# Kernel tuning notes

Hardware: AMD Instinct MI355X
Metric: run time of the kernel (lower is better)

## Reference

```python
import jax, jax.numpy as jnp
import numpy as np

B, N, D = 8, 256, 128   # batch, nodes, feature width
MID, OUT = 128, 128
FEAT = 2 * D            # concat(n_features, hidden)


def _glorot(key, fan_in, fan_out):
    s = (2.0 / (fan_in + fan_out)) ** 0.5
    return jax.random.normal(key, (fan_in, fan_out), dtype=jnp.float32) * s


def setup_inputs() -> dict:
    key = jax.random.key(0)
    ks = jax.random.split(key, 12)
    inp = {
        "hidden": jax.random.normal(ks[0], (B, N, D), dtype=jnp.float32),
        "n_features": jax.random.normal(ks[1], (B, N, D), dtype=jnp.float32),
        "e_features": jax.random.normal(ks[2], (B, N, N, D), dtype=jnp.float32),
        "g_features": jax.random.normal(ks[3], (B, D), dtype=jnp.float32),
        "adj": jax.random.bernoulli(ks[4], 0.5, (B, N, N)).astype(jnp.float32),
        # Linear params (haiku Linear: y = x @ w + b)
        "W1": _glorot(ks[5], FEAT, MID), "b1": jnp.zeros((MID,), jnp.float32),
        "W2": _glorot(ks[6], FEAT, MID), "b2": jnp.zeros((MID,), jnp.float32),
        "We": _glorot(ks[7], D, MID),    "be": jnp.zeros((MID,), jnp.float32),
        "Wg": _glorot(ks[8], D, MID),    "bg": jnp.zeros((MID,), jnp.float32),
        "Wo1": _glorot(ks[9], FEAT, OUT), "bo1": jnp.zeros((OUT,), jnp.float32),
        "Wo2": _glorot(ks[10], MID, OUT), "bo2": jnp.zeros((OUT,), jnp.float32),
    }
    return inp


def reference(hidden, n_features, e_features, g_features, adj,
              W1, b1, W2, b2, We, be, Wg, bg, Wo1, bo1, Wo2, bo2):
    # features: (B, N, 2D)
    features = jnp.concatenate([n_features, hidden], axis=-1)
    msg_1 = features @ W1 + b1              # (B, N, MID)
    msg_2 = features @ W2 + b2              # (B, N, MID)
    msg_e = e_features @ We + be            # (B, N, N, MID)
    msg_g = g_features @ Wg + bg            # (B, MID)
    # broadcast-add: msgs[b, i, j] = msg_1[b, j] + msg_2[b, i] + msg_e[b, i, j] + msg_g[b]
    msgs = (msg_1[:, None, :, :] + msg_2[:, :, None, :]
            + msg_e + msg_g[:, None, None, :])  # (B, N, N, MID)
    # masked max reduction over axis=1 (default reduction=jnp.max branch)
    msgs = jnp.max(msgs * adj[..., None], axis=1)  # (B, N, MID)
    ret = (features @ Wo1 + bo1) + (msgs @ Wo2 + bo2)  # (B, N, OUT)
    return ret
```

## Files before the change

kernel.cpp:

```cpp
#include <hip/hip_runtime.h>
#include <stdint.h>

#define B_   8
#define N_   256
#define D_   128
#define MID_ 128
#define FEAT_ 256

typedef __attribute__((ext_vector_type(4))) float  floatx4;
typedef __attribute__((ext_vector_type(4))) int    intx4;
typedef __attribute__((ext_vector_type(8))) __bf16 bf16x8;

__device__ __forceinline__ floatx4 mfma16(bf16x8 a, bf16x8 b, floatx4 c) {
    return __builtin_amdgcn_mfma_f32_16x16x32_bf16(a, b, c, 0, 0, 0);
}

__device__ __forceinline__ bf16x8 cvt8(floatx4 a, floatx4 b) {
    bf16x8 r;
    r[0] = (__bf16)a[0]; r[1] = (__bf16)a[1]; r[2] = (__bf16)a[2]; r[3] = (__bf16)a[3];
    r[4] = (__bf16)b[0]; r[5] = (__bf16)b[1]; r[6] = (__bf16)b[2]; r[7] = (__bf16)b[3];
    return r;
}

__global__ void __launch_bounds__(256)
kW(const float* __restrict__ W1, const float* __restrict__ W2,
   const float* __restrict__ Wo1, const float* __restrict__ We,
   __bf16* __restrict__ dst) {
    int t = threadIdx.x;
    int g = blockIdx.x * 2 + (t >> 7);
    int m = t & 127;
    const float* src; int kg; int off;
    if (g < 32)      { src = W1;  kg = g;      off = 0; }
    else if (g < 64) { src = W2;  kg = g - 32; off = 32768; }
    else if (g < 96) { src = Wo1; kg = g - 64; off = 65536; }
    else             { src = We;  kg = g - 96; off = 98304; }
    bf16x8 r;
#pragma unroll
    for (int jv = 0; jv < 8; ++jv) r[jv] = (__bf16)src[(kg * 8 + jv) * MID_ + m];
    int base = (((kg >> 2) * 8 + (m >> 4)) * 64 + (kg & 3) * 16 + (m & 15)) * 8;
    *(bf16x8*)&dst[off + base] = r;
}

__global__ void __launch_bounds__(256)
kA(const float* __restrict__ nfeat, const float* __restrict__ hidden,
   const __bf16* __restrict__ Wpre,
   const float* __restrict__ g, const float* __restrict__ Wg,
   const float* __restrict__ bg, const float* __restrict__ b1,
   const float* __restrict__ be, const float* __restrict__ b2,
   const float* __restrict__ bo1, const float* __restrict__ bo2,
   float* __restrict__ C, float* __restrict__ msg2, float* __restrict__ retA) {
    __shared__ __bf16 Wb[8 * 8 * 64 * 8];
    __shared__ float gp_part[2][MID_];
    __shared__ float gp_sh[MID_];
    int t = threadIdx.x;
    int wid = blockIdx.y;
    {
        const intx4* srcW = (const intx4*)(Wpre + (size_t)wid * 32768);
        intx4* dstW = (intx4*)Wb;
#pragma unroll
        for (int it = 0; it < 16; ++it) dstW[t + it * 256] = srcW[t + it * 256];
    }
    int bblk = blockIdx.x >> 2;
    if (wid == 0) {
        int m = t & 127, h = t >> 7;
        const float* gr = g + bblk * D_;
        float a = 0.f;
        for (int k = h * 64; k < h * 64 + 64; ++k)
            a += gr[k] * Wg[k * MID_ + m];
        gp_part[h][m] = a;
    }
    __syncthreads();
    if (wid == 0 && t < 128)
        gp_sh[t] = gp_part[0][t] + gp_part[1][t] + bg[t] + b1[t] + be[t];
    __syncthreads();

    int lane = t & 63, w = t >> 6;
    int n16 = lane & 15, quad = lane >> 4;
    int R = blockIdx.x * 64 + w * 16 + n16;
    const float* frow0 = nfeat  + (size_t)R * D_ + quad * 8;
    const float* frow1 = hidden + (size_t)R * D_ + quad * 8;

    bf16x8 bfrag[8];
#pragma unroll
    for (int ks = 0; ks < 8; ++ks) {
        const float* p = (ks < 4) ? (frow0 + ks * 32) : (frow1 + (ks - 4) * 32);
        floatx4 v0 = *(const floatx4*)p;
        floatx4 v1 = *(const floatx4*)(p + 4);
        bfrag[ks] = cvt8(v0, v1);
    }

    float* outp = (wid == 0) ? C : ((wid == 1) ? msg2 : retA);
#pragma unroll 2
    for (int mt = 0; mt < 8; ++mt) {
        floatx4 acc = (floatx4)0.f;
#pragma unroll
        for (int ks = 0; ks < 8; ++ks) {
            bf16x8 a = *(const bf16x8*)&Wb[((ks * 8 + mt) * 64 + lane) * 8];
            acc = mfma16(a, bfrag[ks], acc);
        }
        int m0 = mt * 16 + quad * 4;
        floatx4 add;
        if (wid == 0)      add = *(const floatx4*)&gp_sh[m0];
        else if (wid == 1) add = *(const floatx4*)&b2[m0];
        else {
            floatx4 x = *(const floatx4*)&bo1[m0];
            floatx4 y = *(const floatx4*)&bo2[m0];
            add = x + y;
        }
        *(floatx4*)&outp[(size_t)R * MID_ + m0] = acc + add;
    }
}

__global__ void __launch_bounds__(256, 4)
kB(const float* __restrict__ e, const __bf16* __restrict__ Wes,
   const float* __restrict__ adj, const float* __restrict__ C,
   const float* __restrict__ msg2, const float* __restrict__ retA,
   const float* __restrict__ Wo2, float* __restrict__ out) {
    __shared__ __bf16 Wb[4 * 8 * 64 * 8];
    __shared__ float C_sh[MID_];
    __shared__ float wmax[4][MID_];
    __shared__ float msgs_sh[MID_];
    __shared__ float part[2][MID_];
    __shared__ unsigned short list_sh[N_];
    __shared__ float aval_sh[N_];
    __shared__ int wcnt[4];

    int t = threadIdx.x;
    int b = blockIdx.x >> 8, j = blockIdx.x & 255;
    int lane = t & 63, w = t >> 6;
    int n16 = lane & 15, quad = lane >> 4;

    {
        const intx4* srcW = (const intx4*)Wes;
        intx4* dstW = (intx4*)Wb;
#pragma unroll
        for (int it = 0; it < 8; ++it) dstW[t + it * 256] = srcW[t + it * 256];
    }
    float av = adj[(size_t)b * N_ * N_ + (size_t)t * N_ + j];
    bool act = (av != 0.f);
    unsigned long long mk = __ballot(act);
    if (lane == 0) wcnt[w] = __popcll(mk);
    if (t < 128) C_sh[t] = C[((size_t)b * N_ + j) * MID_ + t];
    __syncthreads();
    int nact = wcnt[0] + wcnt[1] + wcnt[2] + wcnt[3];
    int base = 0;
    if (w > 0) base += wcnt[0];
    if (w > 1) base += wcnt[1];
    if (w > 2) base += wcnt[2];
    int pos = base + __popcll(mk & ((1ull << lane) - 1ull));
    if (act) { list_sh[pos] = (unsigned short)t; aval_sh[pos] = av; }
    __syncthreads();

    const size_t erow = (size_t)N_ * D_;
    const float* ebase = e + (size_t)b * N_ * N_ * D_ + (size_t)j * D_ + quad * 8;
    const float* m2b   = msg2 + (size_t)b * N_ * MID_;

    floatx4 rm[8];
#pragma unroll
    for (int mt = 0; mt < 8; ++mt) rm[mt] = (floatx4)(-INFINITY);

    int nch = (nact + 15) >> 4;

    int idxn = 0; float awn = 0.f;
    {
        int slot = w * 16 + n16;
        if (w < nch && slot < nact) { idxn = list_sh[slot]; awn = aval_sh[slot]; }
    }
    floatx4 v[8];
    {
        const float* rowp = ebase + (size_t)idxn * erow;
#pragma unroll
        for (int q = 0; q < 4; ++q) {
            v[2 * q]     = *(const floatx4*)(rowp + q * 32);
            v[2 * q + 1] = *(const floatx4*)(rowp + q * 32 + 4);
        }
    }

    for (int c = w; c < nch; c += 4) {
        bf16x8 ef[4];
#pragma unroll
        for (int q = 0; q < 4; ++q) ef[q] = cvt8(v[2 * q], v[2 * q + 1]);
        float aw = awn;
        const float* m2r = m2b + (size_t)idxn * MID_;

        int cn = c + 4;
        idxn = 0; awn = 0.f;
        {
            int slot = cn * 16 + n16;
            if (cn < nch && slot < nact) { idxn = list_sh[slot]; awn = aval_sh[slot]; }
        }
        {
            const float* rowp = ebase + (size_t)idxn * erow;
#pragma unroll
            for (int q = 0; q < 4; ++q) {
                v[2 * q]     = *(const floatx4*)(rowp + q * 32);
                v[2 * q + 1] = *(const floatx4*)(rowp + q * 32 + 4);
            }
        }

#pragma unroll 2
        for (int mt = 0; mt < 8; ++mt) {
            int m0 = mt * 16 + quad * 4;
            floatx4 m2v = *(const floatx4*)&m2r[m0];
            floatx4 acc = *(const floatx4*)&C_sh[m0];
#pragma unroll
            for (int ks = 0; ks < 4; ++ks) {
                bf16x8 aW = *(const bf16x8*)&Wb[((ks * 8 + mt) * 64 + lane) * 8];
                acc = mfma16(aW, ef[ks], acc);
            }
#pragma unroll
            for (int r = 0; r < 4; ++r)
                rm[mt][r] = fmaxf(rm[mt][r], (acc[r] + m2v[r]) * aw);
        }
    }

#pragma unroll
    for (int mt = 0; mt < 8; ++mt) {
#pragma unroll
        for (int r = 0; r < 4; ++r) {
            float vv = rm[mt][r];
            vv = fmaxf(vv, __shfl_xor(vv, 1, 64));
            vv = fmaxf(vv, __shfl_xor(vv, 2, 64));
            vv = fmaxf(vv, __shfl_xor(vv, 4, 64));
            vv = fmaxf(vv, __shfl_xor(vv, 8, 64));
            rm[mt][r] = vv;
        }
    }
    if (n16 == 0) {
#pragma unroll
        for (int mt = 0; mt < 8; ++mt)
            *(floatx4*)&wmax[w][mt * 16 + quad * 4] = rm[mt];
    }
    __syncthreads();

    int m = t & 127, h = t >> 7;
    if (t < 128) {
        float mx = fmaxf(fmaxf(wmax[0][m], wmax[1][m]), fmaxf(wmax[2][m], wmax[3][m]));
        if (nact < 256) mx = fmaxf(mx, 0.f);
        msgs_sh[m] = mx;
    }
    __syncthreads();

    float a2 = 0.f;
    for (int k = h * 64; k < h * 64 + 64; ++k)
        a2 += msgs_sh[k] * Wo2[k * MID_ + m];
    part[h][m] = a2;
    __syncthreads();
    if (t < 128) {
        int R = b * N_ + j;
        out[(size_t)R * MID_ + m] = retA[R * MID_ + m] + part[0][m] + part[1][m];
    }
}

extern "C" void kernel_launch(void* const* d_in, const int* in_sizes, int n_in,
                              void* d_out, int out_size, void* d_ws, size_t ws_size,
                              hipStream_t stream) {
    (void)in_sizes; (void)n_in; (void)out_size; (void)ws_size;
    const float* hidden = (const float*)d_in[0];
    const float* nfeat  = (const float*)d_in[1];
    const float* e      = (const float*)d_in[2];
    const float* g      = (const float*)d_in[3];
    const float* adj    = (const float*)d_in[4];
    const float* W1  = (const float*)d_in[5];
    const float* b1  = (const float*)d_in[6];
    const float* W2  = (const float*)d_in[7];
    const float* b2  = (const float*)d_in[8];
    const float* We  = (const float*)d_in[9];
    const float* be  = (const float*)d_in[10];
    const float* Wg  = (const float*)d_in[11];
    const float* bg  = (const float*)d_in[12];
    const float* Wo1 = (const float*)d_in[13];
    const float* bo1 = (const float*)d_in[14];
    const float* Wo2 = (const float*)d_in[15];
    const float* bo2 = (const float*)d_in[16];
    float* outp = (float*)d_out;

    float* ws = (float*)d_ws;
    __bf16* Wpre = (__bf16*)ws;
    float* C    = ws + 57344;
    float* msg2 = C + 262144;
    float* retA = msg2 + 262144;

    kW<<<56, 256, 0, stream>>>(W1, W2, Wo1, We, Wpre);
    kA<<<dim3(32, 3), 256, 0, stream>>>(nfeat, hidden, Wpre,
                                        g, Wg, bg, b1, be, b2, bo1, bo2,
                                        C, msg2, retA);
    kB<<<2048, 256, 0, stream>>>(e, Wpre + 98304, adj, C, msg2, retA, Wo2, outp);
}
```

Baseline: 399.9 us.

## Restructure edge-chunk loop to pair MFMA chunks and transpose Wo2 for vector loads

```diff
diff --git a/kernel.cpp b/kernel.cpp
--- a/kernel.cpp
+++ b/kernel.cpp
@@ -22,23 +22,70 @@
     return r;
 }
 
+#define LOAD8(v, rp) do { _Pragma("unroll") \
+    for (int q = 0; q < 4; ++q) { \
+        v[2 * q]     = *(const floatx4*)((rp) + q * 32); \
+        v[2 * q + 1] = *(const floatx4*)((rp) + q * 32 + 4); } } while (0)
+
+#define CVT4(ef, v) do { _Pragma("unroll") \
+    for (int q = 0; q < 4; ++q) ef[q] = cvt8(v[2 * q], v[2 * q + 1]); } while (0)
+
+#define MT_PAIR(ef0, aw0, m2r0, ef1, aw1, m2r1) do { _Pragma("unroll 2") \
+    for (int mt = 0; mt < 8; ++mt) { \
+        int m0 = mt * 16 + quad * 4; \
+        floatx4 c4 = *(const floatx4*)&C_sh[m0]; \
+        floatx4 acc0 = c4, acc1 = c4; \
+        _Pragma("unroll") for (int ks = 0; ks < 4; ++ks) { \
+            bf16x8 aW = *(const bf16x8*)&Wb[((ks * 8 + mt) * 64 + lane) * 8]; \
+            acc0 = mfma16(aW, ef0[ks], acc0); \
+            acc1 = mfma16(aW, ef1[ks], acc1); } \
+        floatx4 m20 = *(const floatx4*)&(m2r0)[m0]; \
+        floatx4 m21 = *(const floatx4*)&(m2r1)[m0]; \
+        _Pragma("unroll") for (int r = 0; r < 4; ++r) { \
+            float v0 = (acc0[r] + m20[r]) * (aw0); \
+            float v1 = (acc1[r] + m21[r]) * (aw1); \
+            rm[mt][r] = fmaxf(rm[mt][r], fmaxf(v0, v1)); } } } while (0)
+
+#define MT_SINGLE(ef, aw, m2r) do { _Pragma("unroll 2") \
+    for (int mt = 0; mt < 8; ++mt) { \
+        int m0 = mt * 16 + quad * 4; \
+        floatx4 acc = *(const floatx4*)&C_sh[m0]; \
+        _Pragma("unroll") for (int ks = 0; ks < 4; ++ks) { \
+            bf16x8 aW = *(const bf16x8*)&Wb[((ks * 8 + mt) * 64 + lane) * 8]; \
+            acc = mfma16(aW, ef[ks], acc); } \
+        floatx4 m2v = *(const floatx4*)&(m2r)[m0]; \
+        _Pragma("unroll") for (int r = 0; r < 4; ++r) \
+            rm[mt][r] = fmaxf(rm[mt][r], (acc[r] + m2v[r]) * (aw)); } } while (0)
+
 __global__ void __launch_bounds__(256)
 kW(const float* __restrict__ W1, const float* __restrict__ W2,
    const float* __restrict__ Wo1, const float* __restrict__ We,
-   __bf16* __restrict__ dst) {
+   const float* __restrict__ Wo2,
+   __bf16* __restrict__ dst, float* __restrict__ Wo2T) {
     int t = threadIdx.x;
     int g = blockIdx.x * 2 + (t >> 7);
     int m = t & 127;
-    const float* src; int kg; int off;
-    if (g < 32)      { src = W1;  kg = g;      off = 0; }
-    else if (g < 64) { src = W2;  kg = g - 32; off = 32768; }
-    else if (g < 96) { src = Wo1; kg = g - 64; off = 65536; }
-    else             { src = We;  kg = g - 96; off = 98304; }
-    bf16x8 r;
-#pragma unroll
-    for (int jv = 0; jv < 8; ++jv) r[jv] = (__bf16)src[(kg * 8 + jv) * MID_ + m];
-    int base = (((kg >> 2) * 8 + (m >> 4)) * 64 + (kg & 3) * 16 + (m & 15)) * 8;
-    *(bf16x8*)&dst[off + base] = r;
+    if (g < 112) {
+        const float* src; int kg; int off;
+        if (g < 32)      { src = W1;  kg = g;      off = 0; }
+        else if (g < 64) { src = W2;  kg = g - 32; off = 32768; }
+        else if (g < 96) { src = Wo1; kg = g - 64; off = 65536; }
+        else             { src = We;  kg = g - 96; off = 98304; }
+        bf16x8 r;
+#pragma unroll
+        for (int jv = 0; jv < 8; ++jv) r[jv] = (__bf16)src[(kg * 8 + jv) * MID_ + m];
+        int base = (((kg >> 2) * 8 + (m >> 4)) * 64 + (kg & 3) * 16 + (m & 15)) * 8;
+        *(bf16x8*)&dst[off + base] = r;
+    } else {
+        int kg = g - 112;
+        floatx4 a, b;
+#pragma unroll
+        for (int jv = 0; jv < 4; ++jv) a[jv] = Wo2[(kg * 8 + jv) * MID_ + m];
+#pragma unroll
+        for (int jv = 0; jv < 4; ++jv) b[jv] = Wo2[(kg * 8 + 4 + jv) * MID_ + m];
+        *(floatx4*)&Wo2T[m * MID_ + kg * 8]     = a;
+        *(floatx4*)&Wo2T[m * MID_ + kg * 8 + 4] = b;
+    }
 }
 
 __global__ void __launch_bounds__(256)
@@ -115,7 +162,7 @@
 kB(const float* __restrict__ e, const __bf16* __restrict__ Wes,
    const float* __restrict__ adj, const float* __restrict__ C,
    const float* __restrict__ msg2, const float* __restrict__ retA,
-   const float* __restrict__ Wo2, float* __restrict__ out) {
+   const float* __restrict__ Wo2T, float* __restrict__ out) {
     __shared__ __bf16 Wb[4 * 8 * 64 * 8];
     __shared__ float C_sh[MID_];
     __shared__ float wmax[4][MID_];
@@ -160,57 +207,44 @@
     for (int mt = 0; mt < 8; ++mt) rm[mt] = (floatx4)(-INFINITY);
 
     int nch = (nact + 15) >> 4;
-
-    int idxn = 0; float awn = 0.f;
-    {
-        int slot = w * 16 + n16;
-        if (w < nch && slot < nact) { idxn = list_sh[slot]; awn = aval_sh[slot]; }
-    }
-    floatx4 v[8];
-    {
-        const float* rowp = ebase + (size_t)idxn * erow;
-#pragma unroll
-        for (int q = 0; q < 4; ++q) {
-            v[2 * q]     = *(const floatx4*)(rowp + q * 32);
-            v[2 * q + 1] = *(const floatx4*)(rowp + q * 32 + 4);
-        }
-    }
-
-    for (int c = w; c < nch; c += 4) {
-        bf16x8 ef[4];
-#pragma unroll
-        for (int q = 0; q < 4; ++q) ef[q] = cvt8(v[2 * q], v[2 * q + 1]);
-        float aw = awn;
-        const float* m2r = m2b + (size_t)idxn * MID_;
-
-        int cn = c + 4;
-        idxn = 0; awn = 0.f;
-        {
-            int slot = cn * 16 + n16;
-            if (cn < nch && slot < nact) { idxn = list_sh[slot]; awn = aval_sh[slot]; }
-        }
-        {
-            const float* rowp = ebase + (size_t)idxn * erow;
-#pragma unroll
-            for (int q = 0; q < 4; ++q) {
-                v[2 * q]     = *(const floatx4*)(rowp + q * 32);
-                v[2 * q + 1] = *(const floatx4*)(rowp + q * 32 + 4);
-            }
-        }
-
-#pragma unroll 2
-        for (int mt = 0; mt < 8; ++mt) {
-            int m0 = mt * 16 + quad * 4;
-            floatx4 m2v = *(const floatx4*)&m2r[m0];
-            floatx4 acc = *(const floatx4*)&C_sh[m0];
-#pragma unroll
-            for (int ks = 0; ks < 4; ++ks) {
-                bf16x8 aW = *(const bf16x8*)&Wb[((ks * 8 + mt) * 64 + lane) * 8];
-                acc = mfma16(aW, ef[ks], acc);
-            }
-#pragma unroll
-            for (int r = 0; r < 4; ++r)
-                rm[mt][r] = fmaxf(rm[mt][r], (acc[r] + m2v[r]) * aw);
+    int c0 = w, c1 = w + 4, c2 = w + 8;
+
+    if (c0 < nch) {
+        bool has1 = (c1 < nch), has2 = (c2 < nch);
+        int i0 = 0, i1 = 0, i2 = 0; float aw0 = 0.f, aw1 = 0.f, aw2 = 0.f;
+        { int s = c0 * 16 + n16; if (s < nact) { i0 = list_sh[s]; aw0 = aval_sh[s]; } }
+        if (has1) { int s = c1 * 16 + n16; if (s < nact) { i1 = list_sh[s]; aw1 = aval_sh[s]; } }
+        if (has2) { int s = c2 * 16 + n16; if (s < nact) { i2 = list_sh[s]; aw2 = aval_sh[s]; } }
+
+        floatx4 vA[8], vB[8];
+        bf16x8 ef0[4], ef1[4];
+        const float* r0 = ebase + (size_t)i0 * erow;
+        LOAD8(vA, r0);
+        if (has1) { const float* r1 = ebase + (size_t)i1 * erow; LOAD8(vB, r1); }
+        CVT4(ef0, vA);
+        if (has1) CVT4(ef1, vB);
+        if (has2) { const float* r2 = ebase + (size_t)i2 * erow; LOAD8(vA, r2); }
+
+        const float* m2r0 = m2b + (size_t)i0 * MID_;
+        if (has1) {
+            const float* m2r1 = m2b + (size_t)i1 * MID_;
+            MT_PAIR(ef0, aw0, m2r0, ef1, aw1, m2r1);
+        } else {
+            MT_SINGLE(ef0, aw0, m2r0);
+        }
+        if (has2) {
+            CVT4(ef0, vA);
+            const float* m2r2 = m2b + (size_t)i2 * MID_;
+            MT_SINGLE(ef0, aw2, m2r2);
+        }
+        for (int c = w + 12; c < nch; c += 4) {
+            int s = c * 16 + n16; int idx = 0; float aw = 0.f;
+            if (s < nact) { idx = list_sh[s]; aw = aval_sh[s]; }
+            const float* rp = ebase + (size_t)idx * erow;
+            LOAD8(vA, rp);
+            CVT4(ef0, vA);
+            const float* m2r = m2b + (size_t)idx * MID_;
+            MT_SINGLE(ef0, aw, m2r);
         }
     }
 
@@ -242,8 +276,18 @@
     __syncthreads();
 
     float a2 = 0.f;
-    for (int k = h * 64; k < h * 64 + 64; ++k)
-        a2 += msgs_sh[k] * Wo2[k * MID_ + m];
+    {
+        const float* wrow = Wo2T + (size_t)m * MID_ + h * 64;
+        const float* msr  = &msgs_sh[h * 64];
+#pragma unroll
+        for (int q = 0; q < 16; ++q) {
+            floatx4 wv = *(const floatx4*)(wrow + q * 4);
+            a2 = fmaf(msr[q * 4 + 0], wv[0], a2);
+            a2 = fmaf(msr[q * 4 + 1], wv[1], a2);
+            a2 = fmaf(msr[q * 4 + 2], wv[2], a2);
+            a2 = fmaf(msr[q * 4 + 3], wv[3], a2);
+        }
+    }
     part[h][m] = a2;
     __syncthreads();
     if (t < 128) {
@@ -277,13 +321,14 @@
 
     float* ws = (float*)d_ws;
     __bf16* Wpre = (__bf16*)ws;
-    float* C    = ws + 57344;
-    float* msg2 = C + 262144;
-    float* retA = msg2 + 262144;
-
-    kW<<<56, 256, 0, stream>>>(W1, W2, Wo1, We, Wpre);
+    float* C     = ws + 57344;
+    float* msg2  = C + 262144;
+    float* retA  = msg2 + 262144;
+    float* Wo2T  = retA + 262144;
+
+    kW<<<64, 256, 0, stream>>>(W1, W2, Wo1, We, Wo2, Wpre, Wo2T);
     kA<<<dim3(32, 3), 256, 0, stream>>>(nfeat, hidden, Wpre,
                                         g, Wg, bg, b1, be, b2, bo1, bo2,
                                         C, msg2, retA);
-    kB<<<2048, 256, 0, stream>>>(e, Wpre + 98304, adj, C, msg2, retA, Wo2, outp);
-}
+    kB<<<2048, 256, 0, stream>>>(e, Wpre + 98304, adj, C, msg2, retA, Wo2T, outp);
+}
```

Measured after the change: 403.7 us. No clear change (+1.0%).
